# Kernel optimization log

Hardware: AMD Instinct MI355X
Metric: run time of the kernel (lower is better)

Reference implementation:

```python
import jax, jax.numpy as jnp
import numpy as np

HEADS = 4
DH = 128          # hidden_channels // heads = 512 // 4
HID = 512
R = 5
N1 = 30000        # layer-0 target count (adjs_t[0].size(0))
N2 = 8000         # layer-1 target count (adjs_t[1].size(0))
EPS = 1e-5
NEG_SLOPE = 0.2   # GATConv default leaky_relu slope


def setup_inputs() -> dict:
    key = jax.random.key(0)
    ks = jax.random.split(key, 32)
    N0, E0, E1, DIN, OUT = 120000, 600000, 150000, 768, 153
    s = 0.02
    inp = {}
    inp["x"] = jax.random.normal(ks[0], (N0, DIN), jnp.float32)
    inp["es0"] = jax.random.randint(ks[1], (E0,), 0, N0, jnp.int32)
    inp["ed0"] = jax.random.randint(ks[2], (E0,), 0, N1, jnp.int32)
    inp["et0"] = jax.random.randint(ks[3], (E0,), 0, R, jnp.int32)
    inp["es1"] = jax.random.randint(ks[4], (E1,), 0, N1, jnp.int32)
    inp["ed1"] = jax.random.randint(ks[5], (E1,), 0, N2, jnp.int32)
    inp["et1"] = jax.random.randint(ks[6], (E1,), 0, R, jnp.int32)
    # layer 0 GAT params (stacked over relations)
    inp["W0"] = jax.random.normal(ks[7], (R, DIN, HID), jnp.float32) * s
    inp["as0"] = jax.random.normal(ks[8], (R, HEADS, DH), jnp.float32) * s
    inp["ad0"] = jax.random.normal(ks[9], (R, HEADS, DH), jnp.float32) * s
    inp["b0"] = jnp.zeros((R, HID), jnp.float32)
    inp["Wsk0"] = jax.random.normal(ks[10], (DIN, HID), jnp.float32) * s
    inp["bsk0"] = jnp.zeros((HID,), jnp.float32)
    inp["g0"] = jnp.ones((HID,), jnp.float32)
    inp["be0"] = jnp.zeros((HID,), jnp.float32)
    # layer 1 GAT params
    inp["W1"] = jax.random.normal(ks[11], (R, HID, HID), jnp.float32) * s
    inp["as1"] = jax.random.normal(ks[12], (R, HEADS, DH), jnp.float32) * s
    inp["ad1"] = jax.random.normal(ks[13], (R, HEADS, DH), jnp.float32) * s
    inp["b1"] = jnp.zeros((R, HID), jnp.float32)
    inp["Wsk1"] = jax.random.normal(ks[14], (HID, HID), jnp.float32) * s
    inp["bsk1"] = jnp.zeros((HID,), jnp.float32)
    inp["g1"] = jnp.ones((HID,), jnp.float32)
    inp["be1"] = jnp.zeros((HID,), jnp.float32)
    # output MLP
    inp["Wm1"] = jax.random.normal(ks[15], (HID, HID), jnp.float32) * s
    inp["bm1"] = jnp.zeros((HID,), jnp.float32)
    inp["gm"] = jnp.ones((HID,), jnp.float32)
    inp["bmn"] = jnp.zeros((HID,), jnp.float32)
    inp["Wm2"] = jax.random.normal(ks[16], (HID, OUT), jnp.float32) * s
    inp["bm2"] = jnp.zeros((OUT,), jnp.float32)
    return inp


def _rgat_layer(x, n_dst, esrc, edst, etype, W, a_src, a_dst, b, Wsk, bsk, gamma, beta):
    # skip connection on target nodes (targets are prefix of sources)
    out = x[:n_dst] @ Wsk + bsk
    for j in range(R):  # small fixed relation loop, mirrors per-relation GATConvs
        h = (x @ W[j]).reshape(-1, HEADS, DH)            # shared lin_src == lin_dst
        a_s = jnp.einsum('nhd,hd->nh', h, a_src[j])      # [N, H]
        a_d = jnp.einsum('nhd,hd->nh', h[:n_dst], a_dst[j])
        score = jax.nn.leaky_relu(a_s[esrc] + a_d[edst], NEG_SLOPE)  # [E, H]
        mask = (etype == j)[:, None]
        score = jnp.where(mask, score, -jnp.inf)
        smax = jax.ops.segment_max(score, edst, num_segments=n_dst)
        smax = jnp.where(jnp.isfinite(smax), smax, 0.0)
        ex = jnp.where(mask, jnp.exp(score - smax[edst]), 0.0)       # [E, H]
        denom = jax.ops.segment_sum(ex, edst, num_segments=n_dst)
        alpha = ex / jnp.maximum(denom[edst], 1e-16)
        msg = alpha[..., None] * h[esrc]                              # [E, H, DH]
        agg = jax.ops.segment_sum(msg, edst, num_segments=n_dst)
        out = out + agg.reshape(n_dst, HID) + b[j]
    # BatchNorm1d (training-mode batch stats) + ELU; dropout is identity in reference
    mu = out.mean(0)
    var = out.var(0)
    xn = (out - mu) * jax.lax.rsqrt(var + EPS)
    return jax.nn.elu(gamma * xn + beta)


def reference(x, es0, ed0, et0, es1, ed1, et1,
              W0, as0, ad0, b0, Wsk0, bsk0, g0, be0,
              W1, as1, ad1, b1, Wsk1, bsk1, g1, be1,
              Wm1, bm1, gm, bmn, Wm2, bm2):
    h = _rgat_layer(x, N1, es0, ed0, et0, W0, as0, ad0, b0, Wsk0, bsk0, g0, be0)
    h = _rgat_layer(h, N2, es1, ed1, et1, W1, as1, ad1, b1, Wsk1, bsk1, g1, be1)
    # MLP head: Linear -> BN -> ReLU -> (Dropout) -> Linear
    z = h @ Wm1 + bm1
    mu = z.mean(0)
    var = z.var(0)
    z = jax.nn.relu(gm * ((z - mu) * jax.lax.rsqrt(var + EPS)) + bmn)
    return z @ Wm2 + bm2
```

## Files before the change

kernel.cpp:

```cpp
#include <hip/hip_runtime.h>
#include <math.h>

typedef __bf16 bf16;
typedef __bf16 bf16x4 __attribute__((ext_vector_type(4)));
typedef __bf16 bf16x8 __attribute__((ext_vector_type(8)));
typedef float f32x4 __attribute__((ext_vector_type(4)));

#define M0   120000
#define M0P  120064
#define K0   768
#define HID  512
#define NREL 5
#define N1   30000
#define N1P  30080
#define E0   600000
#define N2   8000
#define N2P  8064
#define E1   150000
#define OUTC 153
#define OUTP 256

#define GLOAD_LDS16(g, s) \
  __builtin_amdgcn_global_load_lds((const __attribute__((address_space(1))) void*)(g), \
                                   (__attribute__((address_space(3))) void*)(s), 16, 0, 0)

template <int MODE>
__global__ __launch_bounds__(256) void gemm_bt(
    const bf16* __restrict__ A, const bf16* __restrict__ Bt, void* __restrict__ Cout,
    int N, int K, int Mv, int Nv, int ldc, const float* __restrict__ bias)
{
  __shared__ __attribute__((aligned(16))) bf16 As[128 * 32];
  __shared__ __attribute__((aligned(16))) bf16 Bs[128 * 32];
  const int tid = threadIdx.x;
  const int w = tid >> 6, l = tid & 63;
  const int tm = blockIdx.x * 128, tn = blockIdx.y * 128;
  const int wm = (w >> 1) * 64, wn = (w & 1) * 64;
  const int lr = l & 15, q = l >> 4;

  f32x4 acc[4][4] = {};

  const int arow = l >> 2;
  const int acol = (l & 3) * 8;
  const bf16* Ag = A + (size_t)tm * K + acol;
  const bf16* Bg = Bt + (size_t)tn * K + acol;

  for (int k0 = 0; k0 < K; k0 += 32) {
#pragma unroll
    for (int i = 0; i < 2; i++) {
      int rb = __builtin_amdgcn_readfirstlane(16 * (2 * w + i));
      GLOAD_LDS16(Ag + (size_t)(rb + arow) * K + k0, As + rb * 32);
      GLOAD_LDS16(Bg + (size_t)(rb + arow) * K + k0, Bs + rb * 32);
    }
    __syncthreads();
    bf16x8 af[4], bfr[4];
#pragma unroll
    for (int i = 0; i < 4; i++)
      af[i] = *(const bf16x8*)&As[(wm + i * 16 + lr) * 32 + q * 8];
#pragma unroll
    for (int jj = 0; jj < 4; jj++)
      bfr[jj] = *(const bf16x8*)&Bs[(wn + jj * 16 + lr) * 32 + q * 8];
#pragma unroll
    for (int i = 0; i < 4; i++)
#pragma unroll
      for (int jj = 0; jj < 4; jj++)
        acc[i][jj] = __builtin_amdgcn_mfma_f32_16x16x32_bf16(af[i], bfr[jj], acc[i][jj], 0, 0, 0);
    __syncthreads();
  }

#pragma unroll
  for (int i = 0; i < 4; i++)
#pragma unroll
    for (int jj = 0; jj < 4; jj++)
#pragma unroll
      for (int r = 0; r < 4; r++) {
        int row = tm + wm + i * 16 + q * 4 + r;
        int col = tn + wn + jj * 16 + lr;
        float v = acc[i][jj][r];
        if (MODE == 1) {
          ((float*)Cout)[(size_t)row * N + col] = v;
        } else {
          if (row < Mv && col < Nv)
            ((float*)Cout)[(size_t)row * ldc + col] = v + bias[col];
        }
      }
}

__global__ __launch_bounds__(256) void gemm_recomb(
    const bf16* __restrict__ A0, size_t sA, const bf16* __restrict__ B0, size_t sB,
    float* __restrict__ C, int K)
{
  __shared__ __attribute__((aligned(16))) bf16 As[128 * 32];
  __shared__ __attribute__((aligned(16))) bf16 Bs[128 * 32];
  const bf16* A = A0 + blockIdx.z * sA;
  const bf16* Bt = B0 + blockIdx.z * sB;
  const int tid = threadIdx.x;
  const int w = tid >> 6, l = tid & 63;
  const int tm = blockIdx.x * 128;
  const int wm = (w >> 1) * 64, wn = (w & 1) * 64;
  const int lr = l & 15, q = l >> 4;

  f32x4 acc[4][4] = {};
  const int arow = l >> 2;
  const int acol = (l & 3) * 8;
  const bf16* Ag = A + (size_t)tm * K + acol;
  const bf16* Bg = Bt + acol;

  for (int k0 = 0; k0 < K; k0 += 32) {
#pragma unroll
    for (int i = 0; i < 2; i++) {
      int rb = __builtin_amdgcn_readfirstlane(16 * (2 * w + i));
      GLOAD_LDS16(Ag + (size_t)(rb + arow) * K + k0, As + rb * 32);
      GLOAD_LDS16(Bg + (size_t)(rb + arow) * K + k0, Bs + rb * 32);
    }
    __syncthreads();
    bf16x8 af[4], bfr[4];
#pragma unroll
    for (int i = 0; i < 4; i++)
      af[i] = *(const bf16x8*)&As[(wm + i * 16 + lr) * 32 + q * 8];
#pragma unroll
    for (int jj = 0; jj < 4; jj++)
      bfr[jj] = *(const bf16x8*)&Bs[(wn + jj * 16 + lr) * 32 + q * 8];
#pragma unroll
    for (int i = 0; i < 4; i++)
#pragma unroll
      for (int jj = 0; jj < 4; jj++)
        acc[i][jj] = __builtin_amdgcn_mfma_f32_16x16x32_bf16(af[i], bfr[jj], acc[i][jj], 0, 0, 0);
    __syncthreads();
  }

#pragma unroll
  for (int i = 0; i < 4; i++)
#pragma unroll
    for (int jj = 0; jj < 4; jj++)
#pragma unroll
      for (int r = 0; r < 4; r++) {
        int row = tm + wm + i * 16 + q * 4 + r;
        int col = blockIdx.z * 128 + wn + jj * 16 + lr;
        C[(size_t)row * 512 + col] += acc[i][jj][r];
      }
}

__global__ void cast_pad_k(const float* __restrict__ src, bf16* __restrict__ dst,
                           long nvalid, long ntot)
{
  long i = ((long)blockIdx.x * 256 + threadIdx.x) * 8;
  if (i >= ntot) return;
  bf16x8 o;
  if (i + 8 <= nvalid) {
    float4 v0 = *(const float4*)(src + i);
    float4 v1 = *(const float4*)(src + i + 4);
    o[0] = (bf16)v0.x; o[1] = (bf16)v0.y; o[2] = (bf16)v0.z; o[3] = (bf16)v0.w;
    o[4] = (bf16)v1.x; o[5] = (bf16)v1.y; o[6] = (bf16)v1.z; o[7] = (bf16)v1.w;
  } else {
#pragma unroll
    for (int t = 0; t < 8; t++)
      o[t] = (i + t < nvalid) ? (bf16)src[i + t] : (bf16)0.f;
  }
  *(bf16x8*)(dst + i) = o;
}

__global__ void transpose_cast_k(const float* __restrict__ W, bf16* __restrict__ Wt,
                                 int K, int Nsrc, int Nvalid)
{
  int n = blockIdx.y;
  int k = blockIdx.x * 256 + threadIdx.x;
  Wt[(size_t)n * K + k] = (n < Nvalid) ? (bf16)W[(size_t)k * Nsrc + n] : (bf16)0.f;
}

__global__ void reorder_brec_k(const bf16* __restrict__ Wt, bf16* __restrict__ Brec, int K)
{
  int i = blockIdx.x * 256 + threadIdx.x;
  int k = i % K;
  int rest = i / K;
  int j = rest % NREL;
  int rest2 = rest / NREL;
  int c = rest2 & 127;
  int h = rest2 >> 7;
  Brec[i] = Wt[((size_t)(j * 512 + h * 128 + c)) * K + k];
}

__global__ void wvec_k(const float* __restrict__ W, const float* __restrict__ a_s,
                       const float* __restrict__ a_d, bf16* __restrict__ wv, int K)
{
  int k = blockIdx.x * 64 + threadIdx.x;
  int col = blockIdx.y;
  float v = 0.f;
  if (col < 40) {
    int j = col >> 3, side = (col >> 2) & 1, h = col & 3;
    const float* Wrow = W + ((size_t)j * K + k) * 512 + h * 128;
    const float* av = (side ? a_d : a_s) + (j * 4 + h) * 128;
    for (int c = 0; c < 128; c++) v += Wrow[c] * av[c];
  }
  wv[(size_t)col * K + k] = (bf16)v;
}

__global__ void fill_i32_k(int* __restrict__ p, int v, int n)
{
  int i = blockIdx.x * 256 + threadIdx.x;
  if (i < n) p[i] = v;
}

__global__ void hist_k(const int* __restrict__ et, const int* __restrict__ ed,
                       int* __restrict__ cnt, int E, int ndst)
{
  int e = blockIdx.x * 256 + threadIdx.x;
  if (e >= E) return;
  atomicAdd(&cnt[et[e] * ndst + ed[e]], 1);
}

__global__ void scan1_k(const int* __restrict__ in, int* __restrict__ out,
                        int* __restrict__ bsums, int n)
{
  __shared__ int sh[256];
  int t = threadIdx.x;
  int i = blockIdx.x * 256 + t;
  int v = (i < n) ? in[i] : 0;
  sh[t] = v;
  __syncthreads();
#pragma unroll
  for (int o = 1; o < 256; o <<= 1) {
    int x = 0;
    if (t >= o) x = sh[t - o];
    __syncthreads();
    if (t >= o) sh[t] += x;
    __syncthreads();
  }
  if (i < n) out[i] = sh[t] - v;
  if (t == 255) bsums[blockIdx.x] = sh[255];
}

__global__ void scan2_k(int* __restrict__ b, int n)
{
  __shared__ int sh[1024];
  int t = threadIdx.x;
  int v = (t < n) ? b[t] : 0;
  sh[t] = v;
  __syncthreads();
#pragma unroll
  for (int o = 1; o < 1024; o <<= 1) {
    int x = 0;
    if (t >= o) x = sh[t - o];
    __syncthreads();
    if (t >= o) sh[t] += x;
    __syncthreads();
  }
  if (t < n) b[t] = sh[t] - v;
}

__global__ void add_off_k(int* __restrict__ out, const int* __restrict__ bscan, int n)
{
  int i = blockIdx.x * 256 + threadIdx.x;
  if (i < n) out[i] += bscan[blockIdx.x];
}

__global__ void copy_cursor_k(int* __restrict__ off, int* __restrict__ cur, int n, int E)
{
  int i = blockIdx.x * 256 + threadIdx.x;
  if (i < n) cur[i] = off[i];
  if (i == 0) off[n] = E;
}

__global__ void scatter_k(const int* __restrict__ es, const int* __restrict__ ed,
                          const int* __restrict__ et, int* __restrict__ cur,
                          int* __restrict__ sorted_src, int E, int ndst)
{
  int e = blockIdx.x * 256 + threadIdx.x;
  if (e >= E) return;
  int pos = atomicAdd(&cur[et[e] * ndst + ed[e]], 1);
  sorted_src[pos] = es[e];
}

template <int K, int CH>
__global__ __launch_bounds__(256) void agg_x_k(
    const int* __restrict__ sorted_src, const int* __restrict__ off,
    const float* __restrict__ scoresbuf, const bf16* __restrict__ X,
    bf16* __restrict__ aggx, int ndst, int nrows)
{
  const int wv = threadIdx.x >> 6;
  const int l  = threadIdx.x & 63;
  const int d  = blockIdx.x * 4 + wv;
  const int j  = blockIdx.y;
  if (d >= ndst) return;
  const int key = j * ndst + d;
  const int beg = off[key], end = off[key + 1];
  const float4 svd = *(const float4*)(scoresbuf + (size_t)d * 128 + j * 8 + 4);

  const int lane_off = l * (CH * 4);

  float den[4] = {0.f, 0.f, 0.f, 0.f};
  float acc[4][CH * 4] = {};

  int p = beg;
  float4 sv0;
  bf16x4 xv0[CH];
  if (p < end) {
    int s0 = sorted_src[p];
    sv0 = *(const float4*)(scoresbuf + (size_t)s0 * 128 + j * 8);
    const bf16* xr = X + (size_t)s0 * K + lane_off;
#pragma unroll
    for (int c = 0; c < CH; c++) xv0[c] = *(const bf16x4*)(xr + c * 4);
  }
  while (p < end) {
    const bool more = (p + 1 < end);
    float4 sv1;
    bf16x4 xv1[CH];
    if (more) {
      int s1 = sorted_src[p + 1];
      sv1 = *(const float4*)(scoresbuf + (size_t)s1 * 128 + j * 8);
      const bf16* xr = X + (size_t)s1 * K + lane_off;
#pragma unroll
      for (int c = 0; c < CH; c++) xv1[c] = *(const bf16x4*)(xr + c * 4);
    }
    float v[4] = {sv0.x + svd.x, sv0.y + svd.y, sv0.z + svd.z, sv0.w + svd.w};
    float e[4];
#pragma unroll
    for (int h = 0; h < 4; h++) {
      float sc = v[h] > 0.f ? v[h] : 0.2f * v[h];
      e[h] = __expf(sc);
      den[h] += e[h];
    }
#pragma unroll
    for (int c = 0; c < CH; c++) {
#pragma unroll
      for (int t = 0; t < 4; t++) {
        float f = (float)xv0[c][t];
#pragma unroll
        for (int h = 0; h < 4; h++)
          acc[h][c * 4 + t] += e[h] * f;
      }
    }
    p++;
    if (more) {
      sv0 = sv1;
#pragma unroll
      for (int c = 0; c < CH; c++) xv0[c] = xv1[c];
    }
  }

#pragma unroll
  for (int h = 0; h < 4; h++) {
    float sc = 1.f / fmaxf(den[h], 1e-16f);
    bf16* orow = aggx + ((size_t)h * nrows + d) * ((size_t)NREL * K) + (size_t)j * K + lane_off;
#pragma unroll
    for (int c = 0; c < CH; c++) {
      bf16x4 o;
#pragma unroll
      for (int t = 0; t < 4; t++) o[t] = (bf16)(acc[h][c * 4 + t] * sc);
      *(bf16x4*)(orow + c * 4) = o;
    }
  }
}

__global__ void bias_combine_k(const float* __restrict__ bsk, const float* __restrict__ brel,
                               float* __restrict__ out, int R)
{
  int c = blockIdx.x * 256 + threadIdx.x;
  if (c >= HID) return;
  float v = bsk[c];
  for (int j = 0; j < R; j++) v += brel[j * HID + c];
  out[c] = v;
}

__global__ void fill_f32_k(float* __restrict__ p, float v, int n)
{
  int i = blockIdx.x * 256 + threadIdx.x;
  if (i < n) p[i] = v;
}

__global__ void bn_stats_k(const float* __restrict__ X, const float* __restrict__ bias,
                           float* __restrict__ sums, float* __restrict__ sumsq, int rows)
{
  int t = threadIdx.x;
  int c0 = t * 2;
  float b0 = bias[c0], b1 = bias[c0 + 1];
  float s0 = 0, s1 = 0, q0 = 0, q1 = 0;
  for (int r = blockIdx.x; r < rows; r += gridDim.x) {
    float2 v = *(const float2*)(X + (size_t)r * HID + c0);
    float v0 = v.x + b0, v1 = v.y + b1;
    s0 += v0; q0 += v0 * v0;
    s1 += v1; q1 += v1 * v1;
  }
  atomicAdd(sums + c0, s0); atomicAdd(sums + c0 + 1, s1);
  atomicAdd(sumsq + c0, q0); atomicAdd(sumsq + c0 + 1, q1);
}

template <int ACT>
__global__ void bn_apply_k(const float* __restrict__ X, const float* __restrict__ bias,
                           const float* __restrict__ sums, const float* __restrict__ sumsq,
                           const float* __restrict__ gamma, const float* __restrict__ beta,
                           bf16* __restrict__ Y, int rows, float invN)
{
  int idx = blockIdx.x * 256 + threadIdx.x;
  int row = idx >> 9, c = idx & 511;
  float y = 0.f;
  if (row < rows) {
    float mu = sums[c] * invN;
    float var = sumsq[c] * invN - mu * mu;
    float v = X[idx] + bias[c];
    float xn = (v - mu) * rsqrtf(var + 1e-5f);
    y = gamma[c] * xn + beta[c];
    y = (ACT == 0) ? (y > 0.f ? y : expm1f(y)) : fmaxf(y, 0.f);
  }
  Y[idx] = (bf16)y;
}

extern "C" void kernel_launch(void* const* d_in, const int* in_sizes, int n_in,
                              void* d_out, int out_size, void* d_ws, size_t ws_size,
                              hipStream_t stream)
{
  const float* x    = (const float*)d_in[0];
  const int*   es0  = (const int*)d_in[1];
  const int*   ed0  = (const int*)d_in[2];
  const int*   et0  = (const int*)d_in[3];
  const int*   es1  = (const int*)d_in[4];
  const int*   ed1  = (const int*)d_in[5];
  const int*   et1  = (const int*)d_in[6];
  const float* W0   = (const float*)d_in[7];
  const float* as0  = (const float*)d_in[8];
  const float* ad0  = (const float*)d_in[9];
  const float* b0   = (const float*)d_in[10];
  const float* Wsk0 = (const float*)d_in[11];
  const float* bsk0 = (const float*)d_in[12];
  const float* g0   = (const float*)d_in[13];
  const float* be0  = (const float*)d_in[14];
  const float* W1   = (const float*)d_in[15];
  const float* as1  = (const float*)d_in[16];
  const float* ad1  = (const float*)d_in[17];
  const float* b1   = (const float*)d_in[18];
  const float* Wsk1 = (const float*)d_in[19];
  const float* bsk1 = (const float*)d_in[20];
  const float* g1   = (const float*)d_in[21];
  const float* be1  = (const float*)d_in[22];
  const float* Wm1  = (const float*)d_in[23];
  const float* bm1  = (const float*)d_in[24];
  const float* gm   = (const float*)d_in[25];
  const float* bmn  = (const float*)d_in[26];
  const float* Wm2  = (const float*)d_in[27];
  const float* bm2  = (const float*)d_in[28];

  char* wsb = (char*)d_ws;
  size_t off = 0;
  auto alloc = [&](size_t bytes) -> char* {
    char* p = wsb + off;
    off = (off + bytes + 255) & ~(size_t)255;
    return p;
  };
  bf16*  Wsk0t  = (bf16*)alloc((size_t)HID * K0 * 2);
  bf16*  Wsk1t  = (bf16*)alloc((size_t)HID * HID * 2);
  bf16*  Wm1t   = (bf16*)alloc((size_t)HID * HID * 2);
  bf16*  Wm2t   = (bf16*)alloc((size_t)OUTP * HID * 2);
  bf16*  W0t    = (bf16*)alloc((size_t)NREL * HID * K0 * 2);
  bf16*  W1t    = (bf16*)alloc((size_t)NREL * HID * HID * 2);
  bf16*  Brec0  = (bf16*)alloc((size_t)4 * 128 * NREL * K0 * 2);
  bf16*  Brec1  = (bf16*)alloc((size_t)4 * 128 * NREL * HID * 2);
  bf16*  wvec0  = (bf16*)alloc((size_t)128 * K0 * 2);
  bf16*  wvec1  = (bf16*)alloc((size_t)128 * HID * 2);
  float* biasb  = (float*)alloc(HID * 4);
  float* statsb = (float*)alloc(1024 * 4);
  int*   offb   = (int*)alloc((size_t)(NREL * N1 + 1) * 4);
  int*   curb   = (int*)alloc((size_t)NREL * N1 * 4);
  int*   bsumsb = (int*)alloc(1024 * 4);
  int*   srtb   = (int*)alloc((size_t)E0 * 4);
  float* out0   = (float*)alloc((size_t)N1P * HID * 4);
  bf16*  h1b    = (bf16*)alloc((size_t)N1P * HID * 2);
  bf16*  h2b    = (bf16*)alloc((size_t)N2P * HID * 2);
  bf16*  zbb    = (bf16*)alloc((size_t)N2P * HID * 2);
  float* out1   = (float*)alloc((size_t)N2P * HID * 4);
  float* zf     = (float*)alloc((size_t)N2P * HID * 4);
  bf16*  xb        = (bf16*)alloc((size_t)M0P * K0 * 2);
  float* scoresbuf = (float*)alloc((size_t)M0P * 128 * 4);
  bf16*  aggx      = (bf16*)alloc((size_t)4 * N1P * NREL * K0 * 2);

  auto build_csr = [&](const int* es, const int* ed, const int* et, int E, int ndst) {
    int nkeys = NREL * ndst;
    int nbE = (E + 255) / 256;
    int nbK = (nkeys + 255) / 256;
    fill_i32_k<<<nbK, 256, 0, stream>>>(curb, 0, nkeys);
    hist_k<<<nbE, 256, 0, stream>>>(et, ed, curb, E, ndst);
    scan1_k<<<nbK, 256, 0, stream>>>(curb, offb, bsumsb, nkeys);
    scan2_k<<<1, 1024, 0, stream>>>(bsumsb, nbK);
    add_off_k<<<nbK, 256, 0, stream>>>(offb, bsumsb, nkeys);
    copy_cursor_k<<<nbK, 256, 0, stream>>>(offb, curb, nkeys, E);
    scatter_k<<<nbE, 256, 0, stream>>>(es, ed, et, curb, srtb, E, ndst);
  };

  cast_pad_k<<<((size_t)M0P * K0 / 8 + 255) / 256, 256, 0, stream>>>(
      x, xb, (long)M0 * K0, (long)M0P * K0);
  for (int j = 0; j < NREL; j++)
    transpose_cast_k<<<dim3(3, 512), 256, 0, stream>>>(
        W0 + (size_t)j * K0 * HID, W0t + (size_t)j * HID * K0, K0, HID, HID);
  transpose_cast_k<<<dim3(3, 512), 256, 0, stream>>>(Wsk0, Wsk0t, K0, HID, HID);
  for (int j = 0; j < NREL; j++)
    transpose_cast_k<<<dim3(2, 512), 256, 0, stream>>>(
        W1 + (size_t)j * HID * HID, W1t + (size_t)j * HID * HID, HID, HID, HID);
  transpose_cast_k<<<dim3(2, 512), 256, 0, stream>>>(Wsk1, Wsk1t, HID, HID, HID);
  transpose_cast_k<<<dim3(2, 512), 256, 0, stream>>>(Wm1, Wm1t, HID, HID, HID);
  transpose_cast_k<<<dim3(2, OUTP), 256, 0, stream>>>(Wm2, Wm2t, HID, OUTC, OUTC);
  reorder_brec_k<<<(4 * 128 * NREL * K0) / 256, 256, 0, stream>>>(W0t, Brec0, K0);
  reorder_brec_k<<<(4 * 128 * NREL * HID) / 256, 256, 0, stream>>>(W1t, Brec1, HID);
  wvec_k<<<dim3(K0 / 64, 128), 64, 0, stream>>>(W0, as0, ad0, wvec0, K0);
  wvec_k<<<dim3(HID / 64, 128), 64, 0, stream>>>(W1, as1, ad1, wvec1, HID);

  {
    const int KT = NREL * K0;
    build_csr(es0, ed0, et0, E0, N1);
    gemm_bt<1><<<dim3(M0P / 128, 1), 256, 0, stream>>>(xb, wvec0, scoresbuf, 128, K0, 0, 0, 0, nullptr);
    gemm_bt<1><<<dim3(N1P / 128, 4), 256, 0, stream>>>(xb, Wsk0t, out0, HID, K0, 0, 0, 0, nullptr);
    for (int h = 0; h < 4; h++)
      fill_i32_k<<<((N1P - N1) * KT * 2 / 4 + 255) / 256, 256, 0, stream>>>(
          (int*)(aggx + ((size_t)h * N1P + N1) * KT), 0, (N1P - N1) * KT / 2);
    agg_x_k<K0, K0 / 256><<<dim3(N1 / 4, NREL), 256, 0, stream>>>(
        srtb, offb, scoresbuf, xb, aggx, N1, N1P);
    gemm_recomb<<<dim3(N1P / 128, 1, 4), 256, 0, stream>>>(
        aggx, (size_t)N1P * KT, Brec0, (size_t)128 * KT, out0, KT);
    bias_combine_k<<<2, 256, 0, stream>>>(bsk0, b0, biasb, NREL);
    fill_f32_k<<<4, 256, 0, stream>>>(statsb, 0.f, 1024);
    bn_stats_k<<<256, 256, 0, stream>>>(out0, biasb, statsb, statsb + 512, N1);
    bn_apply_k<0><<<(N1P * HID) / 256, 256, 0, stream>>>(out0, biasb, statsb, statsb + 512,
                                                         g0, be0, h1b, N1, 1.f / N1);
  }

  {
    const int KT = NREL * HID;
    build_csr(es1, ed1, et1, E1, N2);
    gemm_bt<1><<<dim3(N1P / 128, 1), 256, 0, stream>>>(h1b, wvec1, scoresbuf, 128, HID, 0, 0, 0, nullptr);
    gemm_bt<1><<<dim3(N2P / 128, 4), 256, 0, stream>>>(h1b, Wsk1t, out1, HID, HID, 0, 0, 0, nullptr);
    for (int h = 0; h < 4; h++)
      fill_i32_k<<<((N2P - N2) * KT * 2 / 4 + 255) / 256, 256, 0, stream>>>(
          (int*)(aggx + ((size_t)h * N2P + N2) * KT), 0, (N2P - N2) * KT / 2);
    agg_x_k<HID, HID / 256><<<dim3(N2 / 4, NREL), 256, 0, stream>>>(
        srtb, offb, scoresbuf, h1b, aggx, N2, N2P);
    gemm_recomb<<<dim3(N2P / 128, 1, 4), 256, 0, stream>>>(
        aggx, (size_t)N2P * KT, Brec1, (size_t)128 * KT, out1, KT);
    bias_combine_k<<<2, 256, 0, stream>>>(bsk1, b1, biasb, NREL);
    fill_f32_k<<<4, 256, 0, stream>>>(statsb, 0.f, 1024);
    bn_stats_k<<<256, 256, 0, stream>>>(out1, biasb, statsb, statsb + 512, N2);
    bn_apply_k<0><<<(N2P * HID) / 256, 256, 0, stream>>>(out1, biasb, statsb, statsb + 512,
                                                         g1, be1, h2b, N2, 1.f / N2);
  }

  gemm_bt<1><<<dim3(N2P / 128, 4), 256, 0, stream>>>(h2b, Wm1t, zf, HID, HID, 0, 0, 0, nullptr);
  fill_f32_k<<<4, 256, 0, stream>>>(statsb, 0.f, 1024);
  bn_stats_k<<<256, 256, 0, stream>>>(zf, bm1, statsb, statsb + 512, N2);
  bn_apply_k<1><<<(N2P * HID) / 256, 256, 0, stream>>>(zf, bm1, statsb, statsb + 512,
                                                       gm, bmn, zbb, N2, 1.f / N2);
  gemm_bt<2><<<dim3(N2P / 128, OUTP / 128), 256, 0, stream>>>(
      zbb, Wm2t, d_out, OUTP, HID, N2, OUTC, OUTC, bm2);

  (void)in_sizes; (void)n_in; (void)out_size; (void)ws_size;
}
```

Measured before the change: 1.922 ms.

## Batch four edges per iteration in agg_x_k using direct global-to-LDS row loads

The edge aggregation kernel now handles four incoming edges per loop iteration. Each source feature row is fetched with global_load_lds 16-byte transfers into a per-wave LDS slab, then read back per lane for the accumulation. This aims to put more memory requests in flight per wave than the old one-edge register prefetch, hiding gather latency. In exchange it adds LDS traffic, a full vmcnt wait each batch, and LDS usage that may reduce occupancy.

```diff
diff --git a/kernel.cpp b/kernel.cpp
--- a/kernel.cpp
+++ b/kernel.cpp
@@ -276,6 +276,7 @@
     const float* __restrict__ scoresbuf, const bf16* __restrict__ X,
     bf16* __restrict__ aggx, int ndst, int nrows)
 {
+  __shared__ __attribute__((aligned(16))) bf16 lds[4 * 4 * K];
   const int wv = threadIdx.x >> 6;
   const int l  = threadIdx.x & 63;
   const int d  = blockIdx.x * 4 + wv;
@@ -284,56 +285,63 @@
   const int key = j * ndst + d;
   const int beg = off[key], end = off[key + 1];
   const float4 svd = *(const float4*)(scoresbuf + (size_t)d * 128 + j * 8 + 4);
-
   const int lane_off = l * (CH * 4);
+  const int slab0 = wv * (4 * K);
 
   float den[4] = {0.f, 0.f, 0.f, 0.f};
-  float acc[4][CH * 4] = {};
-
-  int p = beg;
-  float4 sv0;
-  bf16x4 xv0[CH];
-  if (p < end) {
-    int s0 = sorted_src[p];
-    sv0 = *(const float4*)(scoresbuf + (size_t)s0 * 128 + j * 8);
-    const bf16* xr = X + (size_t)s0 * K + lane_off;
-#pragma unroll
-    for (int c = 0; c < CH; c++) xv0[c] = *(const bf16x4*)(xr + c * 4);
-  }
-  while (p < end) {
-    const bool more = (p + 1 < end);
-    float4 sv1;
-    bf16x4 xv1[CH];
-    if (more) {
-      int s1 = sorted_src[p + 1];
-      sv1 = *(const float4*)(scoresbuf + (size_t)s1 * 128 + j * 8);
-      const bf16* xr = X + (size_t)s1 * K + lane_off;
-#pragma unroll
-      for (int c = 0; c < CH; c++) xv1[c] = *(const bf16x4*)(xr + c * 4);
-    }
-    float v[4] = {sv0.x + svd.x, sv0.y + svd.y, sv0.z + svd.z, sv0.w + svd.w};
-    float e[4];
-#pragma unroll
-    for (int h = 0; h < 4; h++) {
-      float sc = v[h] > 0.f ? v[h] : 0.2f * v[h];
-      e[h] = __expf(sc);
-      den[h] += e[h];
-    }
-#pragma unroll
-    for (int c = 0; c < CH; c++) {
-#pragma unroll
-      for (int t = 0; t < 4; t++) {
-        float f = (float)xv0[c][t];
-#pragma unroll
-        for (int h = 0; h < 4; h++)
-          acc[h][c * 4 + t] += e[h] * f;
+  f32x4 acc[4][CH] = {};
+
+  for (int p = beg; p < end; p += 4) {
+    const int rem = end - p;
+    int s[4];
+    float4 sv[4];
+#pragma unroll
+    for (int i = 0; i < 4; i++)
+      if (i < rem) s[i] = sorted_src[p + i];
+#pragma unroll
+    for (int i = 0; i < 4; i++)
+      if (i < rem) sv[i] = *(const float4*)(scoresbuf + (size_t)s[i] * 128 + j * 8);
+#pragma unroll
+    for (int i = 0; i < 4; i++) {
+      if (i < rem) {
+        const bf16* row = X + (size_t)s[i] * K;
+        int ofs = __builtin_amdgcn_readfirstlane(slab0 + i * K);
+        GLOAD_LDS16(row + l * 8, &lds[ofs]);
+        if (K == 768)
+          GLOAD_LDS16(row + 256 + l * 8, &lds[ofs + 256]);
       }
     }
-    p++;
-    if (more) {
-      sv0 = sv1;
-#pragma unroll
-      for (int c = 0; c < CH; c++) xv0[c] = xv1[c];
+    float e[4][4];
+#pragma unroll
+    for (int i = 0; i < 4; i++) {
+      if (i < rem) {
+        float v[4] = {sv[i].x + svd.x, sv[i].y + svd.y, sv[i].z + svd.z, sv[i].w + svd.w};
+#pragma unroll
+        for (int h = 0; h < 4; h++) {
+          float sc = v[h] > 0.f ? v[h] : 0.2f * v[h];
+          e[i][h] = __expf(sc);
+          den[h] += e[i][h];
+        }
+      }
+    }
+    asm volatile("s_waitcnt vmcnt(0)" ::: "memory");
+#pragma unroll
+    for (int i = 0; i < 4; i++) {
+      if (i < rem) {
+        const bf16* xr = &lds[slab0 + i * K + lane_off];
+        f32x4 xf[CH];
+#pragma unroll
+        for (int c = 0; c < CH; c++) {
+          bf16x4 xv = *(const bf16x4*)(xr + c * 4);
+#pragma unroll
+          for (int t = 0; t < 4; t++) xf[c][t] = (float)xv[t];
+        }
+#pragma unroll
+        for (int h = 0; h < 4; h++)
+#pragma unroll
+          for (int c = 0; c < CH; c++)
+            acc[h][c] += e[i][h] * xf[c];
+      }
     }
   }
 
@@ -345,7 +353,7 @@
     for (int c = 0; c < CH; c++) {
       bf16x4 o;
 #pragma unroll
-      for (int t = 0; t < 4; t++) o[t] = (bf16)(acc[h][c * 4 + t] * sc);
+      for (int t = 0; t < 4; t++) o[t] = (bf16)(acc[h][c][t] * sc);
       *(bf16x4*)(orow + c * 4) = o;
     }
   }
```

After: 2.016 ms. 4.9% more time.

## Fuse skip GEMM into recombination GEMM and split aggregation heads across waves

Applied to the files above, without the earlier changes.

The skip-connection GEMM is now computed inside the recombination GEMM kernel as a second K-loop into the same accumulators. The output is written once instead of being read-modify-written, which removes a separate launch and an fp32 round trip of the output. The aggregation kernel now has two waves per destination, each handling two heads instead of four. This halves per-thread accumulator registers to raise occupancy, at the cost of each X row being gathered twice.

```diff
diff --git a/kernel.cpp b/kernel.cpp
--- a/kernel.cpp
+++ b/kernel.cpp
@@ -85,14 +85,16 @@
       }
 }
 
-__global__ __launch_bounds__(256) void gemm_recomb(
+__global__ __launch_bounds__(256) void gemm_recomb_fused(
     const bf16* __restrict__ A0, size_t sA, const bf16* __restrict__ B0, size_t sB,
-    float* __restrict__ C, int K)
+    const bf16* __restrict__ Xs, const bf16* __restrict__ Wskt,
+    float* __restrict__ C, int Kagg, int Ks)
 {
   __shared__ __attribute__((aligned(16))) bf16 As[128 * 32];
   __shared__ __attribute__((aligned(16))) bf16 Bs[128 * 32];
-  const bf16* A = A0 + blockIdx.z * sA;
-  const bf16* Bt = B0 + blockIdx.z * sB;
+  const int z = blockIdx.y;
+  const bf16* A = A0 + (size_t)z * sA;
+  const bf16* Bt = B0 + (size_t)z * sB;
   const int tid = threadIdx.x;
   const int w = tid >> 6, l = tid & 63;
   const int tm = blockIdx.x * 128;
@@ -102,31 +104,43 @@
   f32x4 acc[4][4] = {};
   const int arow = l >> 2;
   const int acol = (l & 3) * 8;
-  const bf16* Ag = A + (size_t)tm * K + acol;
-  const bf16* Bg = Bt + acol;
-
-  for (int k0 = 0; k0 < K; k0 += 32) {
-#pragma unroll
-    for (int i = 0; i < 2; i++) {
-      int rb = __builtin_amdgcn_readfirstlane(16 * (2 * w + i));
-      GLOAD_LDS16(Ag + (size_t)(rb + arow) * K + k0, As + rb * 32);
-      GLOAD_LDS16(Bg + (size_t)(rb + arow) * K + k0, Bs + rb * 32);
-    }
-    __syncthreads();
-    bf16x8 af[4], bfr[4];
-#pragma unroll
-    for (int i = 0; i < 4; i++)
-      af[i] = *(const bf16x8*)&As[(wm + i * 16 + lr) * 32 + q * 8];
-#pragma unroll
-    for (int jj = 0; jj < 4; jj++)
-      bfr[jj] = *(const bf16x8*)&Bs[(wn + jj * 16 + lr) * 32 + q * 8];
-#pragma unroll
-    for (int i = 0; i < 4; i++)
-#pragma unroll
-      for (int jj = 0; jj < 4; jj++)
-        acc[i][jj] = __builtin_amdgcn_mfma_f32_16x16x32_bf16(af[i], bfr[jj], acc[i][jj], 0, 0, 0);
-    __syncthreads();
-  }
+
+#define RECOMB_KSTEP(AgP, BgP, LDK)                                            \
+  {                                                                            \
+    _Pragma("unroll")                                                          \
+    for (int i = 0; i < 2; i++) {                                              \
+      int rb = __builtin_amdgcn_readfirstlane(16 * (2 * w + i));               \
+      GLOAD_LDS16((AgP) + (size_t)(rb + arow) * (LDK) + k0, As + rb * 32);     \
+      GLOAD_LDS16((BgP) + (size_t)(rb + arow) * (LDK) + k0, Bs + rb * 32);     \
+    }                                                                          \
+    __syncthreads();                                                           \
+    bf16x8 af[4], bfr[4];                                                      \
+    _Pragma("unroll")                                                          \
+    for (int i = 0; i < 4; i++)                                                \
+      af[i] = *(const bf16x8*)&As[(wm + i * 16 + lr) * 32 + q * 8];            \
+    _Pragma("unroll")                                                          \
+    for (int jj = 0; jj < 4; jj++)                                             \
+      bfr[jj] = *(const bf16x8*)&Bs[(wn + jj * 16 + lr) * 32 + q * 8];         \
+    _Pragma("unroll")                                                          \
+    for (int i = 0; i < 4; i++)                                                \
+      _Pragma("unroll")                                                        \
+      for (int jj = 0; jj < 4; jj++)                                           \
+        acc[i][jj] = __builtin_amdgcn_mfma_f32_16x16x32_bf16(af[i], bfr[jj],   \
+                                                             acc[i][jj], 0, 0, 0); \
+    __syncthreads();                                                           \
+  }
+
+  {
+    const bf16* Ag = A + (size_t)tm * Kagg + acol;
+    const bf16* Bg = Bt + acol;
+    for (int k0 = 0; k0 < Kagg; k0 += 32) RECOMB_KSTEP(Ag, Bg, Kagg)
+  }
+  {
+    const bf16* Ag = Xs + (size_t)tm * Ks + acol;
+    const bf16* Bg = Wskt + (size_t)(z * 128) * Ks + acol;
+    for (int k0 = 0; k0 < Ks; k0 += 32) RECOMB_KSTEP(Ag, Bg, Ks)
+  }
+#undef RECOMB_KSTEP
 
 #pragma unroll
   for (int i = 0; i < 4; i++)
@@ -135,8 +149,8 @@
 #pragma unroll
       for (int r = 0; r < 4; r++) {
         int row = tm + wm + i * 16 + q * 4 + r;
-        int col = blockIdx.z * 128 + wn + jj * 16 + lr;
-        C[(size_t)row * 512 + col] += acc[i][jj][r];
+        int col = z * 128 + wn + jj * 16 + lr;
+        C[(size_t)row * 512 + col] = acc[i][jj][r];
       }
 }
 
@@ -278,56 +292,54 @@
 {
   const int wv = threadIdx.x >> 6;
   const int l  = threadIdx.x & 63;
-  const int d  = blockIdx.x * 4 + wv;
+  const int d  = blockIdx.x * 2 + (wv >> 1);
+  const int hp = wv & 1;
   const int j  = blockIdx.y;
   if (d >= ndst) return;
   const int key = j * ndst + d;
   const int beg = off[key], end = off[key + 1];
-  const float4 svd = *(const float4*)(scoresbuf + (size_t)d * 128 + j * 8 + 4);
-
+  const float2 svd = *(const float2*)(scoresbuf + (size_t)d * 128 + j * 8 + 4 + hp * 2);
   const int lane_off = l * (CH * 4);
 
-  float den[4] = {0.f, 0.f, 0.f, 0.f};
-  float acc[4][CH * 4] = {};
+  float den0 = 0.f, den1 = 0.f;
+  f32x4 acc0[CH] = {}, acc1[CH] = {};
 
   int p = beg;
-  float4 sv0;
+  float2 sv0;
   bf16x4 xv0[CH];
   if (p < end) {
     int s0 = sorted_src[p];
-    sv0 = *(const float4*)(scoresbuf + (size_t)s0 * 128 + j * 8);
+    sv0 = *(const float2*)(scoresbuf + (size_t)s0 * 128 + j * 8 + hp * 2);
     const bf16* xr = X + (size_t)s0 * K + lane_off;
 #pragma unroll
     for (int c = 0; c < CH; c++) xv0[c] = *(const bf16x4*)(xr + c * 4);
   }
   while (p < end) {
     const bool more = (p + 1 < end);
-    float4 sv1;
+    float2 sv1;
     bf16x4 xv1[CH];
     if (more) {
       int s1 = sorted_src[p + 1];
-      sv1 = *(const float4*)(scoresbuf + (size_t)s1 * 128 + j * 8);
+      sv1 = *(const float2*)(scoresbuf + (size_t)s1 * 128 + j * 8 + hp * 2);
       const bf16* xr = X + (size_t)s1 * K + lane_off;
 #pragma unroll
       for (int c = 0; c < CH; c++) xv1[c] = *(const bf16x4*)(xr + c * 4);
     }
-    float v[4] = {sv0.x + svd.x, sv0.y + svd.y, sv0.z + svd.z, sv0.w + svd.w};
-    float e[4];
-#pragma unroll
-    for (int h = 0; h < 4; h++) {
-      float sc = v[h] > 0.f ? v[h] : 0.2f * v[h];
-      e[h] = __expf(sc);
-      den[h] += e[h];
+    float v0 = sv0.x + svd.x, v1 = sv0.y + svd.y;
+    float t0 = v0 > 0.f ? v0 : 0.2f * v0;
+    float t1 = v1 > 0.f ? v1 : 0.2f * v1;
+    float e0 = __expf(t0), e1 = __expf(t1);
+    den0 += e0; den1 += e1;
+    f32x4 xf[CH];
+#pragma unroll
+    for (int c = 0; c < CH; c++) {
+#pragma unroll
+      for (int t = 0; t < 4; t++) xf[c][t] = (float)xv0[c][t];
     }
 #pragma unroll
     for (int c = 0; c < CH; c++) {
-#pragma unroll
-      for (int t = 0; t < 4; t++) {
-        float f = (float)xv0[c][t];
-#pragma unroll
-        for (int h = 0; h < 4; h++)
-          acc[h][c * 4 + t] += e[h] * f;
-      }
+      acc0[c] += e0 * xf[c];
+      acc1[c] += e1 * xf[c];
     }
     p++;
     if (more) {
@@ -337,16 +349,22 @@
     }
   }
 
-#pragma unroll
-  for (int h = 0; h < 4; h++) {
-    float sc = 1.f / fmaxf(den[h], 1e-16f);
-    bf16* orow = aggx + ((size_t)h * nrows + d) * ((size_t)NREL * K) + (size_t)j * K + lane_off;
+  {
+    float sc0 = 1.f / fmaxf(den0, 1e-16f);
+    float sc1 = 1.f / fmaxf(den1, 1e-16f);
+    const int h0 = hp * 2;
+    bf16* orow0 = aggx + ((size_t)h0 * nrows + d) * ((size_t)NREL * K) + (size_t)j * K + lane_off;
+    bf16* orow1 = aggx + ((size_t)(h0 + 1) * nrows + d) * ((size_t)NREL * K) + (size_t)j * K + lane_off;
 #pragma unroll
     for (int c = 0; c < CH; c++) {
-      bf16x4 o;
-#pragma unroll
-      for (int t = 0; t < 4; t++) o[t] = (bf16)(acc[h][c * 4 + t] * sc);
-      *(bf16x4*)(orow + c * 4) = o;
+      bf16x4 o0, o1;
+#pragma unroll
+      for (int t = 0; t < 4; t++) {
+        o0[t] = (bf16)(acc0[c][t] * sc0);
+        o1[t] = (bf16)(acc1[c][t] * sc1);
+      }
+      *(bf16x4*)(orow0 + c * 4) = o0;
+      *(bf16x4*)(orow1 + c * 4) = o1;
     }
   }
 }
@@ -505,14 +523,13 @@
     const int KT = NREL * K0;
     build_csr(es0, ed0, et0, E0, N1);
     gemm_bt<1><<<dim3(M0P / 128, 1), 256, 0, stream>>>(xb, wvec0, scoresbuf, 128, K0, 0, 0, 0, nullptr);
-    gemm_bt<1><<<dim3(N1P / 128, 4), 256, 0, stream>>>(xb, Wsk0t, out0, HID, K0, 0, 0, 0, nullptr);
     for (int h = 0; h < 4; h++)
       fill_i32_k<<<((N1P - N1) * KT * 2 / 4 + 255) / 256, 256, 0, stream>>>(
           (int*)(aggx + ((size_t)h * N1P + N1) * KT), 0, (N1P - N1) * KT / 2);
-    agg_x_k<K0, K0 / 256><<<dim3(N1 / 4, NREL), 256, 0, stream>>>(
+    agg_x_k<K0, K0 / 256><<<dim3(N1 / 2, NREL), 256, 0, stream>>>(
         srtb, offb, scoresbuf, xb, aggx, N1, N1P);
-    gemm_recomb<<<dim3(N1P / 128, 1, 4), 256, 0, stream>>>(
-        aggx, (size_t)N1P * KT, Brec0, (size_t)128 * KT, out0, KT);
+    gemm_recomb_fused<<<dim3(N1P / 128, 4), 256, 0, stream>>>(
+        aggx, (size_t)N1P * KT, Brec0, (size_t)128 * KT, xb, Wsk0t, out0, KT, K0);
     bias_combine_k<<<2, 256, 0, stream>>>(bsk0, b0, biasb, NREL);
     fill_f32_k<<<4, 256, 0, stream>>>(statsb, 0.f, 1024);
     bn_stats_k<<<256, 256, 0, stream>>>(out0, biasb, statsb, statsb + 512, N1);
@@ -524,14 +541,13 @@
     const int KT = NREL * HID;
     build_csr(es1, ed1, et1, E1, N2);
     gemm_bt<1><<<dim3(N1P / 128, 1), 256, 0, stream>>>(h1b, wvec1, scoresbuf, 128, HID, 0, 0, 0, nullptr);
-    gemm_bt<1><<<dim3(N2P / 128, 4), 256, 0, stream>>>(h1b, Wsk1t, out1, HID, HID, 0, 0, 0, nullptr);
     for (int h = 0; h < 4; h++)
       fill_i32_k<<<((N2P - N2) * KT * 2 / 4 + 255) / 256, 256, 0, stream>>>(
           (int*)(aggx + ((size_t)h * N2P + N2) * KT), 0, (N2P - N2) * KT / 2);
-    agg_x_k<HID, HID / 256><<<dim3(N2 / 4, NREL), 256, 0, stream>>>(
+    agg_x_k<HID, HID / 256><<<dim3(N2 / 2, NREL), 256, 0, stream>>>(
         srtb, offb, scoresbuf, h1b, aggx, N2, N2P);
-    gemm_recomb<<<dim3(N2P / 128, 1, 4), 256, 0, stream>>>(
-        aggx, (size_t)N2P * KT, Brec1, (size_t)128 * KT, out1, KT);
+    gemm_recomb_fused<<<dim3(N2P / 128, 4), 256, 0, stream>>>(
+        aggx, (size_t)N2P * KT, Brec1, (size_t)128 * KT, h1b, Wsk1t, out1, KT, HID);
     bias_combine_k<<<2, 256, 0, stream>>>(bsk1, b1, biasb, NREL);
     fill_f32_k<<<4, 256, 0, stream>>>(statsb, 0.f, 1024);
     bn_stats_k<<<256, 256, 0, stream>>>(out1, biasb, statsb, statsb + 512, N2);
```

Result: slower. 2.001 ms (+4.1%).
